# Kernel tuning notes

Hardware: AMD Instinct MI355X
Metric: run time of the kernel (lower is better)

Reference implementation:

```python
import jax, jax.numpy as jnp
import numpy as np

B, D, S = 16384, 2048, 512      # batch, input_dim, sideinfo_dim
E, H1, H2 = 8, 1024, 512        # subexpert_num, subexpert_unit
EPS = 1e-5                       # BatchNorm eps (torch default)


def setup_inputs() -> dict:
    key = jax.random.key(0)
    ks = jax.random.split(key, 16)
    inp = {
        "input": jax.random.normal(ks[0], (B, D), jnp.float32),
        "sideinfo": jax.random.normal(ks[1], (B, S), jnp.float32),
        # expert layer 1: Linear(D->H1) per expert, batched over E
        "W1": jax.random.normal(ks[2], (E, D, H1), jnp.float32) / np.sqrt(D),
        "b1": jax.random.normal(ks[3], (E, H1), jnp.float32) * 0.01,
        "gamma1": 1.0 + 0.01 * jax.random.normal(ks[4], (E, H1), jnp.float32),
        "beta1": jax.random.normal(ks[5], (E, H1), jnp.float32) * 0.01,
        "mean1": jax.random.normal(ks[6], (E, H1), jnp.float32) * 0.01,
        "var1": jax.random.uniform(ks[7], (E, H1), jnp.float32, 0.5, 1.5),
        # expert layer 2: Linear(H1->H2) per expert
        "W2": jax.random.normal(ks[8], (E, H1, H2), jnp.float32) / np.sqrt(H1),
        "b2": jax.random.normal(ks[9], (E, H2), jnp.float32) * 0.01,
        "gamma2": 1.0 + 0.01 * jax.random.normal(ks[10], (E, H2), jnp.float32),
        "beta2": jax.random.normal(ks[11], (E, H2), jnp.float32) * 0.01,
        "mean2": jax.random.normal(ks[12], (E, H2), jnp.float32) * 0.01,
        "var2": jax.random.uniform(ks[13], (E, H2), jnp.float32, 0.5, 1.5),
        # gate: Linear(S->E) + softmax
        "Wg": jax.random.normal(ks[14], (S, E), jnp.float32) / np.sqrt(S),
        "bg": jax.random.normal(ks[15], (E,), jnp.float32) * 0.01,
    }
    return inp


def _bn(x, gamma, beta, mean, var):
    # eval-mode BatchNorm1d with per-expert running stats; x: [B,E,H]
    return (x - mean) * (gamma * jax.lax.rsqrt(var + EPS)) + beta


def reference(input, sideinfo, W1, b1, gamma1, beta1, mean1, var1,
              W2, b2, gamma2, beta2, mean2, var2, Wg, bg):
    # all E expert MLPs as two batched GEMMs (dropout is identity in eval)
    h = jnp.einsum('bd,edh->beh', input, W1) + b1            # [B,E,H1]
    h = jax.nn.relu(_bn(h, gamma1, beta1, mean1, var1))
    o = jnp.einsum('beh,eho->beo', h, W2) + b2               # [B,E,H2]
    o = jax.nn.relu(_bn(o, gamma2, beta2, mean2, var2))
    gate = jax.nn.softmax(sideinfo @ Wg + bg, axis=1)        # [B,E]
    return jnp.einsum('beo,be->bo', o, gate)                 # [B,H2]
```

## Files before the change

kernel.cpp:

```cpp
#include <hip/hip_runtime.h>
#include <hip/hip_bf16.h>

static constexpr int B_  = 16384;
static constexpr int D_  = 2048;
static constexpr int S_  = 512;
static constexpr int E_  = 8;
static constexpr int H1_ = 1024;
static constexpr int H2_ = 512;
static constexpr float EPS_ = 1e-5f;

typedef __bf16 bf16x8 __attribute__((ext_vector_type(8)));
typedef float  f32x4  __attribute__((ext_vector_type(4)));

static __device__ __forceinline__ unsigned short f2bf(float f) {
    unsigned u = __float_as_uint(f);
    unsigned r = (u + 0x7fffu + ((u >> 16) & 1u)) >> 16;
    return (unsigned short)r;
}


__global__ void cvt_bf16_kernel(const float* __restrict__ in, ushort* __restrict__ out, long n) {
    long i = ((long)blockIdx.x * blockDim.x + threadIdx.x) * 4;
    long stride = (long)gridDim.x * blockDim.x * 4;
    for (; i < n; i += stride) {
        float4 v = *(const float4*)(in + i);
        ushort4 o;
        o.x = f2bf(v.x); o.y = f2bf(v.y); o.z = f2bf(v.z); o.w = f2bf(v.w);
        *(ushort4*)(out + i) = o;
    }
}

__global__ void transpose_cvt_kernel(const float* __restrict__ in, ushort* __restrict__ out,
                                     int R, int C) {
    __shared__ float t[64][65];
    int nbr = R >> 6, nbc = C >> 6;
    int bid = blockIdx.x;
    int e = bid / (nbr * nbc);
    int rem = bid % (nbr * nbc);
    int br = (rem / nbc) << 6, bc = (rem % nbc) << 6;
    const float* ip = in + (size_t)e * R * C;
    ushort* op = out + (size_t)e * R * C;
    int tcol = (threadIdx.x & 15) * 4;
    int trow = threadIdx.x >> 4;
#pragma unroll
    for (int p = 0; p < 4; p++) {
        int r = trow + p * 16;
        float4 v = *(const float4*)(ip + (size_t)(br + r) * C + bc + tcol);
        t[r][tcol + 0] = v.x; t[r][tcol + 1] = v.y; t[r][tcol + 2] = v.z; t[r][tcol + 3] = v.w;
    }
    __syncthreads();
#pragma unroll
    for (int p = 0; p < 4; p++) {
        int c = trow + p * 16;
        ushort4 o;
        o.x = f2bf(t[tcol + 0][c]);
        o.y = f2bf(t[tcol + 1][c]);
        o.z = f2bf(t[tcol + 2][c]);
        o.w = f2bf(t[tcol + 3][c]);
        *(ushort4*)(op + (size_t)(bc + c) * R + br + tcol) = o;
    }
}

__global__ void fold_bn_kernel(const float* __restrict__ gamma, const float* __restrict__ beta,
                               const float* __restrict__ mean, const float* __restrict__ var,
                               const float* __restrict__ bias,
                               float* __restrict__ Sv, float* __restrict__ Tv, int n) {
    int i = blockIdx.x * 256 + threadIdx.x;
    if (i < n) {
        float s = gamma[i] * rsqrtf(var[i] + EPS_);
        Sv[i] = s;
        Tv[i] = (bias[i] - mean[i]) * s + beta[i];
    }
}

__global__ void gate_kernel(const float* __restrict__ side, const float* __restrict__ Wg,
                            const float* __restrict__ bg, float* __restrict__ gate) {
    int wid = threadIdx.x >> 6, lane = threadIdx.x & 63;
    int b = blockIdx.x * 4 + wid;
    const float* sp = side + (size_t)b * S_ + lane * 8;
    float4 v0 = *(const float4*)sp;
    float4 v1 = *(const float4*)(sp + 4);
    float sv[8] = {v0.x, v0.y, v0.z, v0.w, v1.x, v1.y, v1.z, v1.w};
    float acc[E_] = {0,0,0,0,0,0,0,0};
    const float* wrow = Wg + (size_t)(lane * 8) * E_;
#pragma unroll
    for (int j = 0; j < 8; j++) {
        float4 w0 = *(const float4*)(wrow + j * E_);
        float4 w1 = *(const float4*)(wrow + j * E_ + 4);
        acc[0] += sv[j] * w0.x; acc[1] += sv[j] * w0.y;
        acc[2] += sv[j] * w0.z; acc[3] += sv[j] * w0.w;
        acc[4] += sv[j] * w1.x; acc[5] += sv[j] * w1.y;
        acc[6] += sv[j] * w1.z; acc[7] += sv[j] * w1.w;
    }
#pragma unroll
    for (int off = 32; off; off >>= 1)
#pragma unroll
        for (int e = 0; e < E_; e++) acc[e] += __shfl_xor(acc[e], off, 64);
    float m = -1e30f;
#pragma unroll
    for (int e = 0; e < E_; e++) { acc[e] += bg[e]; m = fmaxf(m, acc[e]); }
    float s = 0.f;
#pragma unroll
    for (int e = 0; e < E_; e++) { acc[e] = __expf(acc[e] - m); s += acc[e]; }
    float inv = 1.f / s;
    if (lane < E_) gate[(size_t)b * E_ + lane] = acc[lane] * inv;
}


__device__ __forceinline__ void g2lds16(const void* g, void* l) {
    __builtin_amdgcn_global_load_lds((const __attribute__((address_space(1))) unsigned int*)g,
                                     (__attribute__((address_space(3))) unsigned int*)l,
                                     16, 0, 0);
}

#define BAR()      asm volatile("s_barrier" ::: "memory")
#define WAITVM(n)  asm volatile("s_waitcnt vmcnt(" #n ")" ::: "memory")
#define MFMA(a,b,c) __builtin_amdgcn_mfma_f32_16x16x32_bf16((a),(b),(c),0,0,0)


template<int EPI>
__global__ __launch_bounds__(512, 2)
void gemm8(const ushort* __restrict__ A, const ushort* __restrict__ Bt, long aBatch,
           const float* __restrict__ Sv, const float* __restrict__ Tv,
           ushort* __restrict__ hout, float* __restrict__ outp, const float* __restrict__ gate,
           int M, int N, int K, int tilesN, int tilesM)
{
    extern __shared__ char smem[];

    const int NT  = K >> 6;
    const int tpe = tilesM * tilesN;

    const int nwg = gridDim.x, per = nwg >> 3;
    const int b0  = blockIdx.x;
    const int bid = (b0 & 7) * per + (b0 >> 3);

    const int e   = bid / tpe;
    const int rem = bid % tpe;
    const int tm  = rem / tilesN, tn = rem % tilesN;

    const char* aBase = (const char*)(A + (size_t)e * aBatch + (size_t)tm * 256 * K);
    const char* bBase = (const char*)(Bt + (size_t)e * N * K + (size_t)tn * 256 * K);
    const size_t rowB = (size_t)K * 2;
    const size_t half2 = 64 * rowB;
    const size_t half1 = 128 * rowB;

    const int tid = threadIdx.x, w = tid >> 6, lane = tid & 63;
    const int wm = w >> 2, wn = w & 3;

    const int srow = tid >> 3;
    const int scol_sw = ((tid & 7) * 16) ^ ((srow & 7) << 4);
    const int ldsW = w * 1024;

    const int lr = lane & 15;
    const int cks0 = ((lane >> 4) * 16) ^ ((lane & 7) << 4);
    const int cks1 = (64 + (lane >> 4) * 16) ^ ((lane & 7) << 4);
    const char* rdA0 = smem + 98304 + (wm * 128 + lr) * 128 + cks0;
    const char* rdA1 = smem + 98304 + (wm * 128 + lr) * 128 + cks1;
    const char* rdB0 = smem + (wn * 64 + lr) * 128 + cks0;
    const char* rdB1 = smem + (wn * 64 + lr) * 128 + cks1;

#define STG(gp, ldsoff) do { \
        g2lds16((gp), smem + (ldsoff)); \
        g2lds16((gp) + half2, smem + (ldsoff) + 8192); } while (0)

    const char* ga = aBase + (size_t)srow * rowB + scol_sw;
    const char* gb = bBase + (size_t)srow * rowB + scol_sw;

    f32x4 acc[8][4] = {};
    bf16x8 aC[4], aN[4], bC[4], bN[4];

    int bCur = 0, bN1 = 32768, bN2 = 65536;

    STG(ga,                98304 + 0 + 0     + ldsW);
    STG(ga + half1,        98304 + 0 + 16384 + ldsW);
    STG(gb,                0     + 0     + ldsW);
    STG(gb + half1,        0     + 16384 + ldsW);
    STG(gb + 128,          32768 + 0     + ldsW);
    STG(gb + half1 + 128,  32768 + 16384 + ldsW);
    WAITVM(4);
    BAR();

#pragma unroll
    for (int mf = 0; mf < 4; ++mf) aC[mf] = *(const bf16x8*)(rdA0 + mf * 2048);
#pragma unroll
    for (int nf = 0; nf < 4; ++nf) bC[nf] = *(const bf16x8*)(rdB0 + nf * 2048);

    const char* spA0 = ga + 128;
    const char* spA1 = ga + half1 + 128;
    const char* spB0 = gb + 256;
    const char* spB1 = gb + half1 + 256;

#pragma unroll 2
    for (int t = 0; t < NT; ++t) {
        const int bi    = t & 1;
        const int oRA   = bi * 32768;
        const int oRAN  = (bi ^ 1) * 32768;
        const int oSA   = 98304 + (bi ^ 1) * 32768;
        const bool moreA = (t < NT - 1);
        const bool moreB = (t < NT - 2);

#pragma unroll
        for (int mf = 0; mf < 4; ++mf) aN[mf] = *(const bf16x8*)(rdA0 + oRA + (4 + mf) * 2048);
        if (moreA) {
            STG(spA0, oSA + 0 + ldsW);
            STG(spA1, oSA + 16384 + ldsW);
        }
        __builtin_amdgcn_s_setprio(1);
#pragma unroll
        for (int mf = 0; mf < 4; ++mf)
#pragma unroll
            for (int nf = 0; nf < 4; ++nf)
                acc[mf][nf] = MFMA(aC[mf], bC[nf], acc[mf][nf]);
        __builtin_amdgcn_s_setprio(0);

#pragma unroll
        for (int mf = 0; mf < 4; ++mf) aC[mf] = *(const bf16x8*)(rdA1 + oRA + mf * 2048);
#pragma unroll
        for (int nf = 0; nf < 4; ++nf) bN[nf] = *(const bf16x8*)(rdB1 + bCur + nf * 2048);
        if (moreB) STG(spB0, bN2 + 0 + ldsW);
        __builtin_amdgcn_s_setprio(1);
#pragma unroll
        for (int mf = 0; mf < 4; ++mf)
#pragma unroll
            for (int nf = 0; nf < 4; ++nf)
                acc[4 + mf][nf] = MFMA(aN[mf], bC[nf], acc[4 + mf][nf]);
        __builtin_amdgcn_s_setprio(0);

#pragma unroll
        for (int mf = 0; mf < 4; ++mf) aN[mf] = *(const bf16x8*)(rdA1 + oRA + (4 + mf) * 2048);
        if (moreB) STG(spB1, bN2 + 16384 + ldsW);
        __builtin_amdgcn_s_setprio(1);
#pragma unroll
        for (int mf = 0; mf < 4; ++mf)
#pragma unroll
            for (int nf = 0; nf < 4; ++nf)
                acc[mf][nf] = MFMA(aC[mf], bN[nf], acc[mf][nf]);
        __builtin_amdgcn_s_setprio(0);

        __builtin_amdgcn_s_setprio(1);
#pragma unroll
        for (int mf = 0; mf < 4; ++mf)
#pragma unroll
            for (int nf = 0; nf < 4; ++nf)
                acc[4 + mf][nf] = MFMA(aN[mf], bN[nf], acc[4 + mf][nf]);
        __builtin_amdgcn_s_setprio(0);

        if (moreA) {
            if (moreB) { WAITVM(4); } else { WAITVM(0); }
            BAR();
#pragma unroll
            for (int mf = 0; mf < 4; ++mf) aC[mf] = *(const bf16x8*)(rdA0 + oRAN + mf * 2048);
#pragma unroll
            for (int nf = 0; nf < 4; ++nf) bC[nf] = *(const bf16x8*)(rdB0 + bN1 + nf * 2048);
        }

        spA0 += 128; spA1 += 128; spB0 += 128; spB1 += 128;
        const int tb = bCur; bCur = bN1; bN1 = bN2; bN2 = tb;
    }

    const int rbase = tm * 256 + wm * 128 + (lane >> 4) * 4;
    const int cbase = tn * 256 + wn * 64 + lr;
    if (EPI == 1) {
#pragma unroll
        for (int nf = 0; nf < 4; ++nf) {
            const int col = cbase + nf * 16;
            const float s = Sv[e * N + col];
            const float tt = Tv[e * N + col];
#pragma unroll
            for (int mf = 0; mf < 8; ++mf) {
                const int row0 = rbase + mf * 16;
                f32x4 v = acc[mf][nf];
#pragma unroll
                for (int r = 0; r < 4; ++r) {
                    float x = v[r] * s + tt;
                    x = x > 0.f ? x : 0.f;
                    hout[((size_t)e * M + row0 + r) * N + col] = f2bf(x);
                }
            }
        }
    }
#undef STG
}


__global__ __launch_bounds__(512, 2)
void gemm2e(const ushort* __restrict__ H, const ushort* __restrict__ W2T,
            const float* __restrict__ Sv, const float* __restrict__ Tv,
            const float* __restrict__ gate, float* __restrict__ outp)
{
    extern __shared__ char smem[];

    const int b0 = blockIdx.x;
    const int bid = (b0 & 7) * 32 + (b0 >> 3);
    const int tm = bid >> 1, tn = bid & 1;

    const size_t rowB  = (size_t)H1_ * 2;
    const size_t strAE = (size_t)B_ * H1_ * 2;
    const size_t strBE = (size_t)H2_ * H1_ * 2;
    const size_t half2 = 64 * rowB;
    const size_t halfB = 128 * rowB;

    const int tid = threadIdx.x, w = tid >> 6, lane = tid & 63;
    const int wm = w >> 2, wn = w & 3;

    const int srow = tid >> 3;
    const int scol_sw = ((tid & 7) * 16) ^ ((srow & 7) << 4);
    const int ldsW = w * 1024;

    const int lr = lane & 15;
    const int cks0 = ((lane >> 4) * 16) ^ ((lane & 7) << 4);
    const int cks1 = (64 + (lane >> 4) * 16) ^ ((lane & 7) << 4);
    const char* rdA0 = smem + (wm * 64 + lr) * 128 + cks0;
    const char* rdA1 = smem + (wm * 64 + lr) * 128 + cks1;
    const char* rdB0 = smem + (wn * 64 + lr) * 128 + cks0;
    const char* rdB1 = smem + (wn * 64 + lr) * 128 + cks1;

    const char* ga = (const char*)H + (size_t)tm * 128 * rowB + (size_t)srow * rowB + scol_sw;
    const char* gb = (const char*)W2T + (size_t)tn * 256 * rowB + (size_t)srow * rowB + scol_sw;

#define STG6(gAp, gBp, aOff, bOff) do { \
        g2lds16((gAp),                 smem + (aOff) + 0     + ldsW); \
        g2lds16((gAp) + half2,         smem + (aOff) + 8192  + ldsW); \
        g2lds16((gBp),                 smem + (bOff) + 0     + ldsW); \
        g2lds16((gBp) + half2,         smem + (bOff) + 8192  + ldsW); \
        g2lds16((gBp) + halfB,         smem + (bOff) + 16384 + ldsW); \
        g2lds16((gBp) + halfB + half2, smem + (bOff) + 24576 + ldsW); } while (0)

    f32x4 acc[4][4] = {};
    f32x4 oacc[4][4] = {};
    bf16x8 a0[4], a1[4], b0v[4], b1v[4];

    int aCur = 98304, aN1 = 114688, aN2 = 131072;
    int bCur = 0,     bN1 = 32768,  bN2 = 65536;

    STG6(ga, gb, aCur, bCur);
    STG6(ga + 128, gb + 128, aN1, bN1);
    WAITVM(6);
    BAR();

#pragma unroll
    for (int mf = 0; mf < 4; ++mf) a0[mf] = *(const bf16x8*)(rdA0 + aCur + mf * 2048);
#pragma unroll
    for (int nf = 0; nf < 4; ++nf) b0v[nf] = *(const bf16x8*)(rdB0 + bCur + nf * 2048);

    const int rbase = tm * 128 + wm * 64 + (lane >> 4) * 4;
    const int cbase = tn * 256 + wn * 64 + lr;

    for (int t = 0; t < 128; ++t) {
        const int t2 = t + 2;
        const bool moreS = (t2 < 128);
        const bool moreT = (t < 127);

        const char* gA2 = ga + (size_t)(t2 >> 4) * strAE + (t2 & 15) * 128;
        const char* gB2 = gb + (size_t)(t2 >> 4) * strBE + (t2 & 15) * 128;

#pragma unroll
        for (int mf = 0; mf < 4; ++mf) a1[mf] = *(const bf16x8*)(rdA1 + aCur + mf * 2048);
#pragma unroll
        for (int nf = 0; nf < 4; ++nf) b1v[nf] = *(const bf16x8*)(rdB1 + bCur + nf * 2048);
        if (moreS) STG6(gA2, gB2, aN2, bN2);
        __builtin_amdgcn_s_setprio(1);
#pragma unroll
        for (int mf = 0; mf < 4; ++mf)
#pragma unroll
            for (int nf = 0; nf < 4; ++nf)
                acc[mf][nf] = MFMA(a0[mf], b0v[nf], acc[mf][nf]);
        __builtin_amdgcn_s_setprio(0);

        __builtin_amdgcn_s_setprio(1);
#pragma unroll
        for (int mf = 0; mf < 4; ++mf)
#pragma unroll
            for (int nf = 0; nf < 4; ++nf)
                acc[mf][nf] = MFMA(a1[mf], b1v[nf], acc[mf][nf]);
        __builtin_amdgcn_s_setprio(0);

        if (moreT) {
            if (moreS) { WAITVM(6); } else { WAITVM(0); }
            BAR();
#pragma unroll
            for (int mf = 0; mf < 4; ++mf) a0[mf] = *(const bf16x8*)(rdA0 + aN1 + mf * 2048);
#pragma unroll
            for (int nf = 0; nf < 4; ++nf) b0v[nf] = *(const bf16x8*)(rdB0 + bN1 + nf * 2048);
        }

        if ((t & 15) == 15) {
            const int e = t >> 4;
            float sc[4], tc[4];
#pragma unroll
            for (int nf = 0; nf < 4; ++nf) {
                sc[nf] = Sv[e * H2_ + cbase + nf * 16];
                tc[nf] = Tv[e * H2_ + cbase + nf * 16];
            }
#pragma unroll
            for (int mf = 0; mf < 4; ++mf) {
#pragma unroll
                for (int r = 0; r < 4; ++r) {
                    const int row = rbase + mf * 16 + r;
                    const float g = gate[(size_t)row * E_ + e];
#pragma unroll
                    for (int nf = 0; nf < 4; ++nf) {
                        float x = acc[mf][nf][r] * sc[nf] + tc[nf];
                        x = x > 0.f ? x : 0.f;
                        oacc[mf][nf][r] += g * x;
                    }
                }
            }
#pragma unroll
            for (int mf = 0; mf < 4; ++mf)
#pragma unroll
                for (int nf = 0; nf < 4; ++nf)
                    acc[mf][nf] = (f32x4){0.f, 0.f, 0.f, 0.f};
        }

        const int ta = aCur; aCur = aN1; aN1 = aN2; aN2 = ta;
        const int tb = bCur; bCur = bN1; bN1 = bN2; bN2 = tb;
    }

#pragma unroll
    for (int mf = 0; mf < 4; ++mf) {
#pragma unroll
        for (int r = 0; r < 4; ++r) {
            const int row = rbase + mf * 16 + r;
#pragma unroll
            for (int nf = 0; nf < 4; ++nf)
                outp[(size_t)row * H2_ + cbase + nf * 16] = oacc[mf][nf][r];
        }
    }
#undef STG6
}


extern "C" void kernel_launch(void* const* d_in, const int* in_sizes, int n_in,
                              void* d_out, int out_size, void* d_ws, size_t ws_size,
                              hipStream_t stream) {
    (void)in_sizes; (void)n_in; (void)out_size; (void)ws_size;

    const float* input    = (const float*)d_in[0];
    const float* sideinfo = (const float*)d_in[1];
    const float* W1   = (const float*)d_in[2];
    const float* b1   = (const float*)d_in[3];
    const float* g1   = (const float*)d_in[4];
    const float* be1  = (const float*)d_in[5];
    const float* m1   = (const float*)d_in[6];
    const float* v1   = (const float*)d_in[7];
    const float* W2   = (const float*)d_in[8];
    const float* b2   = (const float*)d_in[9];
    const float* g2   = (const float*)d_in[10];
    const float* be2  = (const float*)d_in[11];
    const float* m2   = (const float*)d_in[12];
    const float* v2   = (const float*)d_in[13];
    const float* Wg   = (const float*)d_in[14];
    const float* bg   = (const float*)d_in[15];

    char* w = (char*)d_ws;
    size_t off = 0;
    auto carve = [&](size_t bytes) {
        void* p = w + off;
        off += (bytes + 255) & ~(size_t)255;
        return p;
    };
    ushort* Abf  = (ushort*)carve((size_t)B_ * D_ * 2);
    ushort* W1T  = (ushort*)carve((size_t)E_ * H1_ * D_ * 2);
    ushort* W2T  = (ushort*)carve((size_t)E_ * H2_ * H1_ * 2);
    ushort* hbuf = (ushort*)carve((size_t)E_ * B_ * H1_ * 2);
    float*  S1   = (float*)carve((size_t)E_ * H1_ * 4);
    float*  T1   = (float*)carve((size_t)E_ * H1_ * 4);
    float*  S2   = (float*)carve((size_t)E_ * H2_ * 4);
    float*  T2   = (float*)carve((size_t)E_ * H2_ * 4);
    float*  gatep = (float*)carve((size_t)B_ * E_ * 4);

    float* outp = (float*)d_out;

    hipFuncSetAttribute(reinterpret_cast<const void*>(&gemm8<1>),
                        hipFuncAttributeMaxDynamicSharedMemorySize, 163840);
    hipFuncSetAttribute(reinterpret_cast<const void*>(&gemm2e),
                        hipFuncAttributeMaxDynamicSharedMemorySize, 147456);

    cvt_bf16_kernel<<<4096, 256, 0, stream>>>(input, Abf, (long)B_ * D_);
    transpose_cvt_kernel<<<E_ * (D_ / 64) * (H1_ / 64), 256, 0, stream>>>(W1, W1T, D_, H1_);
    transpose_cvt_kernel<<<E_ * (H1_ / 64) * (H2_ / 64), 256, 0, stream>>>(W2, W2T, H1_, H2_);
    fold_bn_kernel<<<(E_ * H1_ + 255) / 256, 256, 0, stream>>>(g1, be1, m1, v1, b1, S1, T1, E_ * H1_);
    fold_bn_kernel<<<(E_ * H2_ + 255) / 256, 256, 0, stream>>>(g2, be2, m2, v2, b2, S2, T2, E_ * H2_);
    gate_kernel<<<B_ / 4, 256, 0, stream>>>(sideinfo, Wg, bg, gatep);

    gemm8<1><<<E_ * (B_ / 256) * (H1_ / 256), 512, 163840, stream>>>(
        Abf, W1T, 0L, S1, T1, hbuf, nullptr, nullptr, B_, H1_, D_, H1_ / 256, B_ / 256);

    gemm2e<<<(B_ / 128) * (H2_ / 256), 512, 147456, stream>>>(
        hbuf, W2T, S2, T2, gatep, outp);
}
```

Before: 705.2 us.

## Use 16 waves per block in layer-1 GEMM with smaller per-wave tiles

Layer-1 expert GEMM now launches 1024 threads (16 waves) per 256x256 tile instead of 512, so each wave computes a 64x64 sub-tile with 16 accumulators instead of 128x64 with 32. The staging loads are redistributed across the extra threads, and the software-pipelined register prefetch of fragments is dropped in favour of a simpler load-then-MFMA loop. The aim is more waves to hide latency with lower register pressure, at the cost of less register-level reuse, more LDS reads per MFMA, and no prefetch overlap. Launch bounds of (1024,4) may force heavy register limits or be unsatisfiable with 160KB of LDS per block.

```diff
diff --git a/kernel.cpp b/kernel.cpp
--- a/kernel.cpp
+++ b/kernel.cpp
@@ -119,7 +119,7 @@
 
 
 template<int EPI>
-__global__ __launch_bounds__(512, 2)
+__global__ __launch_bounds__(1024, 4)
 void gemm8(const ushort* __restrict__ A, const ushort* __restrict__ Bt, long aBatch,
            const float* __restrict__ Sv, const float* __restrict__ Tv,
            ushort* __restrict__ hout, float* __restrict__ outp, const float* __restrict__ gate,
@@ -141,7 +141,6 @@
     const char* aBase = (const char*)(A + (size_t)e * aBatch + (size_t)tm * 256 * K);
     const char* bBase = (const char*)(Bt + (size_t)e * N * K + (size_t)tn * 256 * K);
     const size_t rowB = (size_t)K * 2;
-    const size_t half2 = 64 * rowB;
     const size_t half1 = 128 * rowB;
 
     const int tid = threadIdx.x, w = tid >> 6, lane = tid & 63;
@@ -154,111 +153,75 @@
     const int lr = lane & 15;
     const int cks0 = ((lane >> 4) * 16) ^ ((lane & 7) << 4);
     const int cks1 = (64 + (lane >> 4) * 16) ^ ((lane & 7) << 4);
-    const char* rdA0 = smem + 98304 + (wm * 128 + lr) * 128 + cks0;
-    const char* rdA1 = smem + 98304 + (wm * 128 + lr) * 128 + cks1;
+    const char* rdA0 = smem + 98304 + (wm * 64 + lr) * 128 + cks0;
+    const char* rdA1 = smem + 98304 + (wm * 64 + lr) * 128 + cks1;
     const char* rdB0 = smem + (wn * 64 + lr) * 128 + cks0;
     const char* rdB1 = smem + (wn * 64 + lr) * 128 + cks1;
 
-#define STG(gp, ldsoff) do { \
-        g2lds16((gp), smem + (ldsoff)); \
-        g2lds16((gp) + half2, smem + (ldsoff) + 8192); } while (0)
+#define STG2T(gp, ldsoff) do { \
+        g2lds16((gp), smem + (ldsoff) + ldsW); \
+        g2lds16((gp) + half1, smem + (ldsoff) + 16384 + ldsW); } while (0)
 
     const char* ga = aBase + (size_t)srow * rowB + scol_sw;
     const char* gb = bBase + (size_t)srow * rowB + scol_sw;
 
-    f32x4 acc[8][4] = {};
-    bf16x8 aC[4], aN[4], bC[4], bN[4];
+    f32x4 acc[4][4] = {};
+    bf16x8 a[4], b[4];
 
     int bCur = 0, bN1 = 32768, bN2 = 65536;
 
-    STG(ga,                98304 + 0 + 0     + ldsW);
-    STG(ga + half1,        98304 + 0 + 16384 + ldsW);
-    STG(gb,                0     + 0     + ldsW);
-    STG(gb + half1,        0     + 16384 + ldsW);
-    STG(gb + 128,          32768 + 0     + ldsW);
-    STG(gb + half1 + 128,  32768 + 16384 + ldsW);
-    WAITVM(4);
+    STG2T(ga,       98304);
+    STG2T(gb,       0);
+    STG2T(gb + 128, 32768);
+    WAITVM(2);
     BAR();
 
-#pragma unroll
-    for (int mf = 0; mf < 4; ++mf) aC[mf] = *(const bf16x8*)(rdA0 + mf * 2048);
-#pragma unroll
-    for (int nf = 0; nf < 4; ++nf) bC[nf] = *(const bf16x8*)(rdB0 + nf * 2048);
-
-    const char* spA0 = ga + 128;
-    const char* spA1 = ga + half1 + 128;
-    const char* spB0 = gb + 256;
-    const char* spB1 = gb + half1 + 256;
-
-#pragma unroll 2
+    const char* spA = ga + 128;
+    const char* spB = gb + 256;
+
     for (int t = 0; t < NT; ++t) {
         const int bi    = t & 1;
         const int oRA   = bi * 32768;
-        const int oRAN  = (bi ^ 1) * 32768;
         const int oSA   = 98304 + (bi ^ 1) * 32768;
         const bool moreA = (t < NT - 1);
         const bool moreB = (t < NT - 2);
 
 #pragma unroll
-        for (int mf = 0; mf < 4; ++mf) aN[mf] = *(const bf16x8*)(rdA0 + oRA + (4 + mf) * 2048);
+        for (int mf = 0; mf < 4; ++mf) a[mf] = *(const bf16x8*)(rdA0 + oRA + mf * 2048);
+#pragma unroll
+        for (int nf = 0; nf < 4; ++nf) b[nf] = *(const bf16x8*)(rdB0 + bCur + nf * 2048);
+        if (moreA) STG2T(spA, oSA);
+        __builtin_amdgcn_s_setprio(1);
+#pragma unroll
+        for (int mf = 0; mf < 4; ++mf)
+#pragma unroll
+            for (int nf = 0; nf < 4; ++nf)
+                acc[mf][nf] = MFMA(a[mf], b[nf], acc[mf][nf]);
+        __builtin_amdgcn_s_setprio(0);
+
+#pragma unroll
+        for (int mf = 0; mf < 4; ++mf) a[mf] = *(const bf16x8*)(rdA1 + oRA + mf * 2048);
+#pragma unroll
+        for (int nf = 0; nf < 4; ++nf) b[nf] = *(const bf16x8*)(rdB1 + bCur + nf * 2048);
+        if (moreB) STG2T(spB, bN2);
+        __builtin_amdgcn_s_setprio(1);
+#pragma unroll
+        for (int mf = 0; mf < 4; ++mf)
+#pragma unroll
+            for (int nf = 0; nf < 4; ++nf)
+                acc[mf][nf] = MFMA(a[mf], b[nf], acc[mf][nf]);
+        __builtin_amdgcn_s_setprio(0);
+
         if (moreA) {
-            STG(spA0, oSA + 0 + ldsW);
-            STG(spA1, oSA + 16384 + ldsW);
+            if (moreB) { WAITVM(2); } else { WAITVM(0); }
+            BAR();
         }
-        __builtin_amdgcn_s_setprio(1);
-#pragma unroll
-        for (int mf = 0; mf < 4; ++mf)
-#pragma unroll
-            for (int nf = 0; nf < 4; ++nf)
-                acc[mf][nf] = MFMA(aC[mf], bC[nf], acc[mf][nf]);
-        __builtin_amdgcn_s_setprio(0);
-
-#pragma unroll
-        for (int mf = 0; mf < 4; ++mf) aC[mf] = *(const bf16x8*)(rdA1 + oRA + mf * 2048);
-#pragma unroll
-        for (int nf = 0; nf < 4; ++nf) bN[nf] = *(const bf16x8*)(rdB1 + bCur + nf * 2048);
-        if (moreB) STG(spB0, bN2 + 0 + ldsW);
-        __builtin_amdgcn_s_setprio(1);
-#pragma unroll
-        for (int mf = 0; mf < 4; ++mf)
-#pragma unroll
-            for (int nf = 0; nf < 4; ++nf)
-                acc[4 + mf][nf] = MFMA(aN[mf], bC[nf], acc[4 + mf][nf]);
-        __builtin_amdgcn_s_setprio(0);
-
-#pragma unroll
-        for (int mf = 0; mf < 4; ++mf) aN[mf] = *(const bf16x8*)(rdA1 + oRA + (4 + mf) * 2048);
-        if (moreB) STG(spB1, bN2 + 16384 + ldsW);
-        __builtin_amdgcn_s_setprio(1);
-#pragma unroll
-        for (int mf = 0; mf < 4; ++mf)
-#pragma unroll
-            for (int nf = 0; nf < 4; ++nf)
-                acc[mf][nf] = MFMA(aC[mf], bN[nf], acc[mf][nf]);
-        __builtin_amdgcn_s_setprio(0);
-
-        __builtin_amdgcn_s_setprio(1);
-#pragma unroll
-        for (int mf = 0; mf < 4; ++mf)
-#pragma unroll
-            for (int nf = 0; nf < 4; ++nf)
-                acc[4 + mf][nf] = MFMA(aN[mf], bN[nf], acc[4 + mf][nf]);
-        __builtin_amdgcn_s_setprio(0);
-
-        if (moreA) {
-            if (moreB) { WAITVM(4); } else { WAITVM(0); }
-            BAR();
-#pragma unroll
-            for (int mf = 0; mf < 4; ++mf) aC[mf] = *(const bf16x8*)(rdA0 + oRAN + mf * 2048);
-#pragma unroll
-            for (int nf = 0; nf < 4; ++nf) bC[nf] = *(const bf16x8*)(rdB0 + bN1 + nf * 2048);
-        }
-
-        spA0 += 128; spA1 += 128; spB0 += 128; spB1 += 128;
+
+        spA += 128; spB += 128;
         const int tb = bCur; bCur = bN1; bN1 = bN2; bN2 = tb;
     }
 
-    const int rbase = tm * 256 + wm * 128 + (lane >> 4) * 4;
+    const int rbase = tm * 256 + wm * 64 + (lane >> 4) * 4;
     const int cbase = tn * 256 + wn * 64 + lr;
     if (EPI == 1) {
 #pragma unroll
@@ -267,7 +230,7 @@
             const float s = Sv[e * N + col];
             const float tt = Tv[e * N + col];
 #pragma unroll
-            for (int mf = 0; mf < 8; ++mf) {
+            for (int mf = 0; mf < 4; ++mf) {
                 const int row0 = rbase + mf * 16;
                 f32x4 v = acc[mf][nf];
 #pragma unroll
@@ -279,7 +242,7 @@
             }
         }
     }
-#undef STG
+#undef STG2T
 }
 
 
@@ -484,7 +447,7 @@
     fold_bn_kernel<<<(E_ * H2_ + 255) / 256, 256, 0, stream>>>(g2, be2, m2, v2, b2, S2, T2, E_ * H2_);
     gate_kernel<<<B_ / 4, 256, 0, stream>>>(sideinfo, Wg, bg, gatep);
 
-    gemm8<1><<<E_ * (B_ / 256) * (H1_ / 256), 512, 163840, stream>>>(
+    gemm8<1><<<E_ * (B_ / 256) * (H1_ / 256), 1024, 163840, stream>>>(
         Abf, W1T, 0L, S1, T1, hbuf, nullptr, nullptr, B_, H1_, D_, H1_ / 256, B_ / 256);
 
     gemm2e<<<(B_ / 128) * (H2_ / 256), 512, 147456, stream>>>(
```

Measured after the change: 695.9 us (median of 3 runs). Within noise of the previous version (-1.3%).
